# Kernel tuning notes

Hardware: AMD Instinct MI355X
Metric: run time of the kernel (lower is better)

The kernel has to match this reference:

```python
import jax, jax.numpy as jnp
import numpy as np

H = 16
HEAD_DIM = 64
LORA_RANK = 32
LORA_ALPHA = 1.0


def _lora_linear(x, W, A, B):
    # torch Linear: y = x @ W.T ; LoRA side path: x @ A @ B * (alpha/rank)
    return x @ W.T + (x @ A) @ B * (LORA_ALPHA / LORA_RANK)


def setup_inputs() -> dict:
    key = jax.random.key(0)
    ks = jax.random.split(key, 8)
    B, S, D = 2, 2048, 1024
    x = jax.random.normal(ks[0], (B, S, D), dtype=jnp.float32)
    # ALiBi-style bias per head with causal mask baked in (combined bias)
    alibi_bias = jax.random.normal(ks[1], (H, S, S), dtype=jnp.float32)
    pad_mask = jnp.zeros((B, 1, 1, S), dtype=jnp.float32)
    W_qkv = jax.random.normal(ks[2], (3 * D, D), dtype=jnp.float32) * 0.02
    A_qkv = jax.random.normal(ks[3], (D, LORA_RANK), dtype=jnp.float32) * 0.02
    B_qkv = jax.random.normal(ks[4], (LORA_RANK, 3 * D), dtype=jnp.float32) * 0.02
    W_out = jax.random.normal(ks[5], (D, D), dtype=jnp.float32) * 0.02
    A_out = jax.random.normal(ks[6], (D, LORA_RANK), dtype=jnp.float32) * 0.02
    B_out = jax.random.normal(ks[7], (LORA_RANK, D), dtype=jnp.float32) * 0.02
    return {"x": x, "alibi_bias": alibi_bias, "pad_mask": pad_mask,
            "W_qkv": W_qkv, "A_qkv": A_qkv, "B_qkv": B_qkv,
            "W_out": W_out, "A_out": A_out, "B_out": B_out}


def reference(x, alibi_bias, pad_mask, W_qkv, A_qkv, B_qkv, W_out, A_out, B_out):
    Bsz, S, D = x.shape
    qkv = _lora_linear(x, W_qkv, A_qkv, B_qkv)              # [B,S,3D]
    qkv = qkv.reshape(Bsz, S, 3, H, HEAD_DIM)
    q = jnp.transpose(qkv[:, :, 0], (0, 2, 1, 3))           # [B,H,S,hd]
    k = jnp.transpose(qkv[:, :, 1], (0, 2, 1, 3))
    v = jnp.transpose(qkv[:, :, 2], (0, 2, 1, 3))
    scores = jnp.einsum('bhqd,bhkd->bhqk', q, k) / jnp.sqrt(jnp.float32(HEAD_DIM))
    scores = scores + alibi_bias[None] + pad_mask           # [B,H,S,S]
    weights = jax.nn.softmax(scores, axis=-1)
    # dropout: eval mode (training=False) -> identity
    attn = jnp.einsum('bhqk,bhkd->bhqd', weights, v)        # [B,H,S,hd]
    attn = jnp.transpose(attn, (0, 2, 1, 3)).reshape(Bsz, S, D)
    return _lora_linear(attn, W_out, A_out, B_out)
```

## Files before the change

kernel.cpp:

```cpp
#include <hip/hip_runtime.h>

#define H_ 16
#define HD_ 64
#define S_ 2048
#define D_ 1024
#define B_ 2
#define R_ 32
#define M_ 4096
#define N3_ 3072

typedef __attribute__((ext_vector_type(8))) short short8;
typedef __attribute__((ext_vector_type(4))) float f32x4;
typedef unsigned short u16;
typedef __attribute__((ext_vector_type(4))) unsigned short u16x4;

__device__ inline u16 f2bf(float f) {
  unsigned u = __float_as_uint(f);
  u += 0x7fff + ((u >> 16) & 1);
  return (u16)(u >> 16);
}

__global__ void fold_kernel(const float* __restrict__ W,
                            const float* __restrict__ A,
                            const float* __restrict__ Bm,
                            u16* __restrict__ out, int OUT, int IN) {
  int idx = blockIdx.x * 256 + threadIdx.x;
  int o = idx / IN;
  int i = idx - o * IN;
  float s = 0.f;
#pragma unroll
  for (int r = 0; r < R_; ++r) s += A[i * R_ + r] * Bm[r * OUT + o];
  out[idx] = f2bf(W[idx] + s * (1.0f / 32.0f));
}

__global__ void cvt_kernel(const float* __restrict__ x, u16* __restrict__ xb) {
  int i = (blockIdx.x * 256 + threadIdx.x) * 4;
  const float4 v = *(const float4*)(x + i);
  u16x4 o = {f2bf(v.x), f2bf(v.y), f2bf(v.z), f2bf(v.w)};
  *(u16x4*)(xb + i) = o;
}

template <int EPI>
__global__ __launch_bounds__(256) void gemm_bf16(
    const u16* __restrict__ X, const u16* __restrict__ Wb,
    float* __restrict__ Yf, u16* __restrict__ Qb, u16* __restrict__ Kb,
    u16* __restrict__ Vtb, int M, int N, int K) {
  __shared__ u16 As[128][40];
  __shared__ u16 Bs[128][40];
  const int t = threadIdx.x;
  const int lane = t & 63;
  const int w = t >> 6;
  const int quad = lane >> 4;
  const int l = lane & 15;
  const int wh = w >> 1;
  const int ww = w & 1;
  const int bm = blockIdx.y * 128;
  const int bn = blockIdx.x * 128;
  const int srow = t >> 1;
  const int soff = (t & 1) * 16;
  const u16* Xp = X + (size_t)(bm + srow) * K + soff;
  const u16* Wp = Wb + (size_t)(bn + srow) * K + soff;
  f32x4 acc[4][4];
#pragma unroll
  for (int i = 0; i < 4; ++i)
#pragma unroll
    for (int j = 0; j < 4; ++j) acc[i][j] = (f32x4){0.f, 0.f, 0.f, 0.f};

  for (int k0 = 0; k0 < K; k0 += 32) {
    const short8 xa = *(const short8*)(Xp + k0);
    const short8 xc = *(const short8*)(Xp + k0 + 8);
    const short8 wa = *(const short8*)(Wp + k0);
    const short8 wc = *(const short8*)(Wp + k0 + 8);
    __syncthreads();
    *(short8*)&As[srow][soff] = xa;
    *(short8*)&As[srow][soff + 8] = xc;
    *(short8*)&Bs[srow][soff] = wa;
    *(short8*)&Bs[srow][soff + 8] = wc;
    __syncthreads();
    short8 af[4], bf[4];
#pragma unroll
    for (int mt = 0; mt < 4; ++mt)
      af[mt] = *(const short8*)&As[wh * 64 + mt * 16 + l][quad * 8];
#pragma unroll
    for (int nt = 0; nt < 4; ++nt)
      bf[nt] = *(const short8*)&Bs[ww * 64 + nt * 16 + l][quad * 8];
#pragma unroll
    for (int mt = 0; mt < 4; ++mt)
#pragma unroll
      for (int nt = 0; nt < 4; ++nt)
        acc[mt][nt] = __builtin_amdgcn_mfma_f32_16x16x32_bf16(
            af[mt], bf[nt], acc[mt][nt], 0, 0, 0);
  }
#pragma unroll
  for (int mt = 0; mt < 4; ++mt) {
#pragma unroll
    for (int nt = 0; nt < 4; ++nt) {
      const int m0 = bm + wh * 64 + mt * 16 + quad * 4;
      const int n = bn + ww * 64 + nt * 16 + l;
      if (EPI == 0) {
#pragma unroll
        for (int r = 0; r < 4; ++r)
          Yf[(size_t)(m0 + r) * N + n] = acc[mt][nt][r];
      } else {
        const int b = m0 >> 11;
        const int s0 = m0 & 2047;
        const int part = n >> 10;
        const int h = (n & 1023) >> 6;
        const int d = n & 63;
        if (part == 0) {
#pragma unroll
          for (int r = 0; r < 4; ++r)
            Qb[((size_t)(b * 16 + h) * 2048 + s0 + r) * 64 + d] =
                f2bf(acc[mt][nt][r]);
        } else if (part == 1) {
#pragma unroll
          for (int r = 0; r < 4; ++r)
            Kb[((size_t)(b * 16 + h) * 2048 + s0 + r) * 64 + d] =
                f2bf(acc[mt][nt][r]);
        } else {
          u16x4 pv = {f2bf(acc[mt][nt][0]), f2bf(acc[mt][nt][1]),
                      f2bf(acc[mt][nt][2]), f2bf(acc[mt][nt][3])};
          *(u16x4*)(Vtb + ((size_t)(b * 16 + h) * 64 + d) * 2048 + s0) = pv;
        }
      }
    }
  }
}

__global__ __launch_bounds__(256) void attn_mfma(
    const u16* __restrict__ Qb, const u16* __restrict__ Kb,
    const u16* __restrict__ Vtb, const float* __restrict__ alibi,
    const float* __restrict__ pad, u16* __restrict__ ctxb) {
  __shared__ u16 KL[64][72];
  __shared__ u16 VL[64][72];
  __shared__ u16 PL[4][32][72];
  const int t = threadIdx.x;
  const int lane = t & 63;
  const int w = t >> 6;
  const int quad = lane >> 4;
  const int l = lane & 15;
  const int b = blockIdx.x;
  const int q0 = blockIdx.y * 128;
  const int h = blockIdx.z;
  const int bh = b * 16 + h;
  const int srow = t >> 2;
  const int sq = (t & 3) * 16;

  short8 qf[2][2];
#pragma unroll
  for (int mt = 0; mt < 2; ++mt)
#pragma unroll
    for (int kq = 0; kq < 2; ++kq)
      qf[mt][kq] = *(const short8*)(Qb +
          ((size_t)bh * 2048 + q0 + w * 32 + mt * 16 + l) * 64 + kq * 32 +
          quad * 8);

  f32x4 Ou[2][4];
  float mrun[2][4], lrun[2][4];
#pragma unroll
  for (int mt = 0; mt < 2; ++mt) {
#pragma unroll
    for (int r = 0; r < 4; ++r) { mrun[mt][r] = -1e30f; lrun[mt][r] = 0.f; }
#pragma unroll
    for (int dn = 0; dn < 4; ++dn) Ou[mt][dn] = (f32x4){0.f, 0.f, 0.f, 0.f};
  }

  const u16* Kg = Kb + ((size_t)bh * 2048) * 64;
  const u16* Vg = Vtb + ((size_t)bh * 64) * 2048;

  for (int kt = 0; kt < S_ / 64; ++kt) {
    const int k0 = kt * 64;
    const short8 kv0 = *(const short8*)(Kg + (size_t)(k0 + srow) * 64 + sq);
    const short8 kv1 = *(const short8*)(Kg + (size_t)(k0 + srow) * 64 + sq + 8);
    const short8 vv0 = *(const short8*)(Vg + (size_t)srow * 2048 + k0 + sq);
    const short8 vv1 = *(const short8*)(Vg + (size_t)srow * 2048 + k0 + sq + 8);
    __syncthreads();
    *(short8*)&KL[srow][sq] = kv0;
    *(short8*)&KL[srow][sq + 8] = kv1;
    *(short8*)&VL[srow][sq] = vv0;
    *(short8*)&VL[srow][sq + 8] = vv1;
    __syncthreads();

    short8 kf[4][2];
#pragma unroll
    for (int nt = 0; nt < 4; ++nt)
#pragma unroll
      for (int kq = 0; kq < 2; ++kq)
        kf[nt][kq] = *(const short8*)&KL[nt * 16 + l][kq * 32 + quad * 8];
    f32x4 sc[2][4];
#pragma unroll
    for (int mt = 0; mt < 2; ++mt)
#pragma unroll
      for (int nt = 0; nt < 4; ++nt) {
        f32x4 c = {0.f, 0.f, 0.f, 0.f};
        c = __builtin_amdgcn_mfma_f32_16x16x32_bf16(qf[mt][0], kf[nt][0], c, 0, 0, 0);
        c = __builtin_amdgcn_mfma_f32_16x16x32_bf16(qf[mt][1], kf[nt][1], c, 0, 0, 0);
        sc[mt][nt] = c;
      }

    float padv[4];
#pragma unroll
    for (int nt = 0; nt < 4; ++nt) padv[nt] = pad[(size_t)b * S_ + k0 + nt * 16 + l];
#pragma unroll
    for (int mt = 0; mt < 2; ++mt)
#pragma unroll
      for (int nt = 0; nt < 4; ++nt) {
        const float* ap = alibi +
            ((size_t)h * S_ + q0 + w * 32 + mt * 16 + quad * 4) * S_ + k0 +
            nt * 16 + l;
#pragma unroll
        for (int r = 0; r < 4; ++r)
          sc[mt][nt][r] = fmaf(sc[mt][nt][r], 0.125f,
                               ap[(size_t)r * S_] + padv[nt]);
      }

#pragma unroll
    for (int mt = 0; mt < 2; ++mt) {
#pragma unroll
      for (int r = 0; r < 4; ++r) {
        float rm = fmaxf(fmaxf(sc[mt][0][r], sc[mt][1][r]),
                         fmaxf(sc[mt][2][r], sc[mt][3][r]));
#pragma unroll
        for (int off = 1; off < 16; off <<= 1)
          rm = fmaxf(rm, __shfl_xor(rm, off, 16));
        const float mnew = fmaxf(mrun[mt][r], rm);
        const float alpha = __expf(mrun[mt][r] - mnew);
        mrun[mt][r] = mnew;
        float rs = 0.f;
#pragma unroll
        for (int nt = 0; nt < 4; ++nt) {
          const float e = __expf(sc[mt][nt][r] - mnew);
          sc[mt][nt][r] = e;
          rs += e;
        }
#pragma unroll
        for (int off = 1; off < 16; off <<= 1) rs += __shfl_xor(rs, off, 16);
        lrun[mt][r] = lrun[mt][r] * alpha + rs;
#pragma unroll
        for (int dn = 0; dn < 4; ++dn) Ou[mt][dn][r] *= alpha;
      }
    }

#pragma unroll
    for (int mt = 0; mt < 2; ++mt)
#pragma unroll
      for (int nt = 0; nt < 4; ++nt)
#pragma unroll
        for (int r = 0; r < 4; ++r)
          PL[w][mt * 16 + quad * 4 + r][nt * 16 + l] = f2bf(sc[mt][nt][r]);

    short8 vf[4][2], pf[2][2];
#pragma unroll
    for (int dn = 0; dn < 4; ++dn)
#pragma unroll
      for (int kq = 0; kq < 2; ++kq)
        vf[dn][kq] = *(const short8*)&VL[dn * 16 + l][kq * 32 + quad * 8];
#pragma unroll
    for (int mt = 0; mt < 2; ++mt)
#pragma unroll
      for (int kq = 0; kq < 2; ++kq)
        pf[mt][kq] = *(const short8*)&PL[w][mt * 16 + l][kq * 32 + quad * 8];
#pragma unroll
    for (int mt = 0; mt < 2; ++mt)
#pragma unroll
      for (int dn = 0; dn < 4; ++dn) {
        Ou[mt][dn] = __builtin_amdgcn_mfma_f32_16x16x32_bf16(
            pf[mt][0], vf[dn][0], Ou[mt][dn], 0, 0, 0);
        Ou[mt][dn] = __builtin_amdgcn_mfma_f32_16x16x32_bf16(
            pf[mt][1], vf[dn][1], Ou[mt][dn], 0, 0, 0);
      }
  }

#pragma unroll
  for (int mt = 0; mt < 2; ++mt) {
#pragma unroll
    for (int r = 0; r < 4; ++r) {
      const float inv = 1.0f / lrun[mt][r];
      const int s = q0 + w * 32 + mt * 16 + quad * 4 + r;
#pragma unroll
      for (int dn = 0; dn < 4; ++dn)
        ctxb[((size_t)b * 2048 + s) * 1024 + h * 64 + dn * 16 + l] =
            f2bf(Ou[mt][dn][r] * inv);
    }
  }
}

extern "C" void kernel_launch(void* const* d_in, const int* in_sizes, int n_in,
                              void* d_out, int out_size, void* d_ws,
                              size_t ws_size, hipStream_t stream) {
  const float* x     = (const float*)d_in[0];
  const float* alibi = (const float*)d_in[1];
  const float* pad   = (const float*)d_in[2];
  const float* W_qkv = (const float*)d_in[3];
  const float* A_qkv = (const float*)d_in[4];
  const float* B_qkv = (const float*)d_in[5];
  const float* W_out = (const float*)d_in[6];
  const float* A_out = (const float*)d_in[7];
  const float* B_out = (const float*)d_in[8];
  float* out = (float*)d_out;

  u16* ws = (u16*)d_ws;
  u16* xb    = ws;
  u16* weffq = xb + (size_t)M_ * D_;
  u16* weffo = weffq + (size_t)N3_ * D_;
  u16* Qb    = weffo + (size_t)D_ * D_;
  u16* Kb    = Qb + (size_t)M_ * D_;
  u16* Vtb   = Kb + (size_t)M_ * D_;
  u16* ctxb  = Vtb + (size_t)M_ * D_;

  fold_kernel<<<(N3_ * D_) / 256, 256, 0, stream>>>(W_qkv, A_qkv, B_qkv, weffq,
                                                    N3_, D_);
  fold_kernel<<<(D_ * D_) / 256, 256, 0, stream>>>(W_out, A_out, B_out, weffo,
                                                   D_, D_);
  cvt_kernel<<<(M_ * D_) / 1024, 256, 0, stream>>>(x, xb);
  gemm_bf16<1><<<dim3(N3_ / 128, M_ / 128), 256, 0, stream>>>(
      xb, weffq, nullptr, Qb, Kb, Vtb, M_, N3_, D_);
  attn_mfma<<<dim3(B_, S_ / 128, H_), 256, 0, stream>>>(Qb, Kb, Vtb, alibi,
                                                        pad, ctxb);
  gemm_bf16<0><<<dim3(D_ / 128, M_ / 128), 256, 0, stream>>>(
      ctxb, weffo, out, nullptr, nullptr, nullptr, M_, D_, D_);
}
```

Before: 625.8 us.

## Share alibi loads across batches in attention and use direct global-to-LDS loads in GEMM

The attention kernel now gives each block both batch elements for one head and a 64-query tile, so each alibi value is loaded once and reused for both batches. Alibi for the next key tile is prefetched into registers. K and V are read straight from global memory into registers instead of being staged through shared memory, which removes the per-tile barriers. The GEMM now uses global_load_lds to copy tiles into unpadded shared memory, which may add LDS bank conflicts on the fragment reads, and without LDS staging each wave reloads the same K/V tile, raising global/cache traffic.

Result: slower. 732.4 us (+17.0%).

```diff
diff --git a/kernel.cpp b/kernel.cpp
--- a/kernel.cpp
+++ b/kernel.cpp
@@ -20,6 +20,12 @@
   return (u16)(u >> 16);
 }
 
+__device__ __forceinline__ void glds16(const u16* g, u16* lds) {
+  __builtin_amdgcn_global_load_lds(
+      (const __attribute__((address_space(1))) unsigned int*)g,
+      (__attribute__((address_space(3))) unsigned int*)lds, 16, 0, 0);
+}
+
 __global__ void fold_kernel(const float* __restrict__ W,
                             const float* __restrict__ A,
                             const float* __restrict__ Bm,
@@ -45,8 +51,8 @@
     const u16* __restrict__ X, const u16* __restrict__ Wb,
     float* __restrict__ Yf, u16* __restrict__ Qb, u16* __restrict__ Kb,
     u16* __restrict__ Vtb, int M, int N, int K) {
-  __shared__ u16 As[128][40];
-  __shared__ u16 Bs[128][40];
+  __shared__ u16 As[128 * 32];
+  __shared__ u16 Bs[128 * 32];
   const int t = threadIdx.x;
   const int lane = t & 63;
   const int w = t >> 6;
@@ -56,10 +62,16 @@
   const int ww = w & 1;
   const int bm = blockIdx.y * 128;
   const int bn = blockIdx.x * 128;
-  const int srow = t >> 1;
-  const int soff = (t & 1) * 16;
-  const u16* Xp = X + (size_t)(bm + srow) * K + soff;
-  const u16* Wp = Wb + (size_t)(bn + srow) * K + soff;
+  const int srow0 = 2 * w * 16 + (lane >> 2);
+  const int scol = (lane & 3) * 8;
+  const u16* gA = X + (size_t)(bm + srow0) * K + scol;
+  const u16* gB = Wb + (size_t)(bn + srow0) * K + scol;
+  const size_t segK = (size_t)16 * K;
+  u16* lA0 = As + 2 * w * 512;
+  u16* lA1 = lA0 + 512;
+  u16* lB0 = Bs + 2 * w * 512;
+  u16* lB1 = lB0 + 512;
+
   f32x4 acc[4][4];
 #pragma unroll
   for (int i = 0; i < 4; ++i)
@@ -67,23 +79,19 @@
     for (int j = 0; j < 4; ++j) acc[i][j] = (f32x4){0.f, 0.f, 0.f, 0.f};
 
   for (int k0 = 0; k0 < K; k0 += 32) {
-    const short8 xa = *(const short8*)(Xp + k0);
-    const short8 xc = *(const short8*)(Xp + k0 + 8);
-    const short8 wa = *(const short8*)(Wp + k0);
-    const short8 wc = *(const short8*)(Wp + k0 + 8);
     __syncthreads();
-    *(short8*)&As[srow][soff] = xa;
-    *(short8*)&As[srow][soff + 8] = xc;
-    *(short8*)&Bs[srow][soff] = wa;
-    *(short8*)&Bs[srow][soff + 8] = wc;
+    glds16(gA + k0, lA0);
+    glds16(gA + k0 + segK, lA1);
+    glds16(gB + k0, lB0);
+    glds16(gB + k0 + segK, lB1);
     __syncthreads();
     short8 af[4], bf[4];
 #pragma unroll
     for (int mt = 0; mt < 4; ++mt)
-      af[mt] = *(const short8*)&As[wh * 64 + mt * 16 + l][quad * 8];
+      af[mt] = *(const short8*)&As[(wh * 64 + mt * 16 + l) * 32 + quad * 8];
 #pragma unroll
     for (int nt = 0; nt < 4; ++nt)
-      bf[nt] = *(const short8*)&Bs[ww * 64 + nt * 16 + l][quad * 8];
+      bf[nt] = *(const short8*)&Bs[(ww * 64 + nt * 16 + l) * 32 + quad * 8];
 #pragma unroll
     for (int mt = 0; mt < 4; ++mt)
 #pragma unroll
@@ -131,158 +139,153 @@
     const u16* __restrict__ Qb, const u16* __restrict__ Kb,
     const u16* __restrict__ Vtb, const float* __restrict__ alibi,
     const float* __restrict__ pad, u16* __restrict__ ctxb) {
-  __shared__ u16 KL[64][72];
-  __shared__ u16 VL[64][72];
-  __shared__ u16 PL[4][32][72];
+  __shared__ u16 PL[4][16][72];
   const int t = threadIdx.x;
   const int lane = t & 63;
   const int w = t >> 6;
   const int quad = lane >> 4;
   const int l = lane & 15;
-  const int b = blockIdx.x;
-  const int q0 = blockIdx.y * 128;
-  const int h = blockIdx.z;
-  const int bh = b * 16 + h;
-  const int srow = t >> 2;
-  const int sq = (t & 3) * 16;
+  const int q0 = blockIdx.x * 64;
+  const int h = blockIdx.y;
+  const int qw = q0 + w * 16;
 
   short8 qf[2][2];
 #pragma unroll
-  for (int mt = 0; mt < 2; ++mt)
+  for (int b = 0; b < 2; ++b)
 #pragma unroll
     for (int kq = 0; kq < 2; ++kq)
-      qf[mt][kq] = *(const short8*)(Qb +
-          ((size_t)bh * 2048 + q0 + w * 32 + mt * 16 + l) * 64 + kq * 32 +
+      qf[b][kq] = *(const short8*)(
+          Qb + ((size_t)(b * 16 + h) * 2048 + qw + l) * 64 + kq * 32 +
           quad * 8);
 
   f32x4 Ou[2][4];
   float mrun[2][4], lrun[2][4];
 #pragma unroll
-  for (int mt = 0; mt < 2; ++mt) {
-#pragma unroll
-    for (int r = 0; r < 4; ++r) { mrun[mt][r] = -1e30f; lrun[mt][r] = 0.f; }
-#pragma unroll
-    for (int dn = 0; dn < 4; ++dn) Ou[mt][dn] = (f32x4){0.f, 0.f, 0.f, 0.f};
+  for (int b = 0; b < 2; ++b) {
+#pragma unroll
+    for (int r = 0; r < 4; ++r) { mrun[b][r] = -1e30f; lrun[b][r] = 0.f; }
+#pragma unroll
+    for (int dn = 0; dn < 4; ++dn) Ou[b][dn] = (f32x4){0.f, 0.f, 0.f, 0.f};
   }
 
-  const u16* Kg = Kb + ((size_t)bh * 2048) * 64;
-  const u16* Vg = Vtb + ((size_t)bh * 64) * 2048;
+  const float* ap0 = alibi + ((size_t)h * S_ + qw + quad * 4) * S_ + l;
+  float alc[4][4];
+#pragma unroll
+  for (int nt = 0; nt < 4; ++nt)
+#pragma unroll
+    for (int r = 0; r < 4; ++r)
+      alc[nt][r] = ap0[(size_t)r * S_ + nt * 16];
+
+  const u16* Kg0 = Kb + (size_t)h * 2048 * 64;
+  const u16* Vg0 = Vtb + (size_t)h * 64 * 2048;
+  const size_t bstride = (size_t)16 * 2048 * 64;
 
   for (int kt = 0; kt < S_ / 64; ++kt) {
     const int k0 = kt * 64;
-    const short8 kv0 = *(const short8*)(Kg + (size_t)(k0 + srow) * 64 + sq);
-    const short8 kv1 = *(const short8*)(Kg + (size_t)(k0 + srow) * 64 + sq + 8);
-    const short8 vv0 = *(const short8*)(Vg + (size_t)srow * 2048 + k0 + sq);
-    const short8 vv1 = *(const short8*)(Vg + (size_t)srow * 2048 + k0 + sq + 8);
-    __syncthreads();
-    *(short8*)&KL[srow][sq] = kv0;
-    *(short8*)&KL[srow][sq + 8] = kv1;
-    *(short8*)&VL[srow][sq] = vv0;
-    *(short8*)&VL[srow][sq + 8] = vv1;
-    __syncthreads();
-
-    short8 kf[4][2];
-#pragma unroll
-    for (int nt = 0; nt < 4; ++nt)
-#pragma unroll
-      for (int kq = 0; kq < 2; ++kq)
-        kf[nt][kq] = *(const short8*)&KL[nt * 16 + l][kq * 32 + quad * 8];
-    f32x4 sc[2][4];
-#pragma unroll
-    for (int mt = 0; mt < 2; ++mt)
+    float aln[4][4];
+    if (kt < S_ / 64 - 1) {
+#pragma unroll
+      for (int nt = 0; nt < 4; ++nt)
+#pragma unroll
+        for (int r = 0; r < 4; ++r)
+          aln[nt][r] = ap0[(size_t)r * S_ + k0 + 64 + nt * 16];
+    }
+    float padv[2][4];
+#pragma unroll
+    for (int b = 0; b < 2; ++b)
+#pragma unroll
+      for (int nt = 0; nt < 4; ++nt)
+        padv[b][nt] = pad[(size_t)b * S_ + k0 + nt * 16 + l];
+
+#pragma unroll
+    for (int b = 0; b < 2; ++b) {
+      const u16* Kg = Kg0 + (size_t)b * bstride + (size_t)k0 * 64;
+      const u16* Vg = Vg0 + (size_t)b * bstride;
+      short8 kf[4][2];
+#pragma unroll
+      for (int nt = 0; nt < 4; ++nt)
+#pragma unroll
+        for (int kq = 0; kq < 2; ++kq)
+          kf[nt][kq] = *(const short8*)(Kg + (size_t)(nt * 16 + l) * 64 +
+                                        kq * 32 + quad * 8);
+      f32x4 sc[4];
 #pragma unroll
       for (int nt = 0; nt < 4; ++nt) {
         f32x4 c = {0.f, 0.f, 0.f, 0.f};
-        c = __builtin_amdgcn_mfma_f32_16x16x32_bf16(qf[mt][0], kf[nt][0], c, 0, 0, 0);
-        c = __builtin_amdgcn_mfma_f32_16x16x32_bf16(qf[mt][1], kf[nt][1], c, 0, 0, 0);
-        sc[mt][nt] = c;
+        c = __builtin_amdgcn_mfma_f32_16x16x32_bf16(qf[b][0], kf[nt][0], c, 0, 0, 0);
+        c = __builtin_amdgcn_mfma_f32_16x16x32_bf16(qf[b][1], kf[nt][1], c, 0, 0, 0);
+        sc[nt] = c;
       }
-
-    float padv[4];
-#pragma unroll
-    for (int nt = 0; nt < 4; ++nt) padv[nt] = pad[(size_t)b * S_ + k0 + nt * 16 + l];
-#pragma unroll
-    for (int mt = 0; mt < 2; ++mt)
-#pragma unroll
-      for (int nt = 0; nt < 4; ++nt) {
-        const float* ap = alibi +
-            ((size_t)h * S_ + q0 + w * 32 + mt * 16 + quad * 4) * S_ + k0 +
-            nt * 16 + l;
+#pragma unroll
+      for (int nt = 0; nt < 4; ++nt)
 #pragma unroll
         for (int r = 0; r < 4; ++r)
-          sc[mt][nt][r] = fmaf(sc[mt][nt][r], 0.125f,
-                               ap[(size_t)r * S_] + padv[nt]);
-      }
-
-#pragma unroll
-    for (int mt = 0; mt < 2; ++mt) {
+          sc[nt][r] = fmaf(sc[nt][r], 0.125f, alc[nt][r] + padv[b][nt]);
 #pragma unroll
       for (int r = 0; r < 4; ++r) {
-        float rm = fmaxf(fmaxf(sc[mt][0][r], sc[mt][1][r]),
-                         fmaxf(sc[mt][2][r], sc[mt][3][r]));
+        float rm = fmaxf(fmaxf(sc[0][r], sc[1][r]), fmaxf(sc[2][r], sc[3][r]));
 #pragma unroll
         for (int off = 1; off < 16; off <<= 1)
           rm = fmaxf(rm, __shfl_xor(rm, off, 16));
-        const float mnew = fmaxf(mrun[mt][r], rm);
-        const float alpha = __expf(mrun[mt][r] - mnew);
-        mrun[mt][r] = mnew;
+        const float mnew = fmaxf(mrun[b][r], rm);
+        const float alpha = __expf(mrun[b][r] - mnew);
+        mrun[b][r] = mnew;
         float rs = 0.f;
 #pragma unroll
         for (int nt = 0; nt < 4; ++nt) {
-          const float e = __expf(sc[mt][nt][r] - mnew);
-          sc[mt][nt][r] = e;
+          const float e = __expf(sc[nt][r] - mnew);
+          sc[nt][r] = e;
           rs += e;
         }
 #pragma unroll
         for (int off = 1; off < 16; off <<= 1) rs += __shfl_xor(rs, off, 16);
-        lrun[mt][r] = lrun[mt][r] * alpha + rs;
-#pragma unroll
-        for (int dn = 0; dn < 4; ++dn) Ou[mt][dn][r] *= alpha;
+        lrun[b][r] = lrun[b][r] * alpha + rs;
+#pragma unroll
+        for (int dn = 0; dn < 4; ++dn) Ou[b][dn][r] *= alpha;
       }
-    }
-
-#pragma unroll
-    for (int mt = 0; mt < 2; ++mt)
 #pragma unroll
       for (int nt = 0; nt < 4; ++nt)
 #pragma unroll
         for (int r = 0; r < 4; ++r)
-          PL[w][mt * 16 + quad * 4 + r][nt * 16 + l] = f2bf(sc[mt][nt][r]);
-
-    short8 vf[4][2], pf[2][2];
-#pragma unroll
-    for (int dn = 0; dn < 4; ++dn)
+          PL[w][quad * 4 + r][nt * 16 + l] = f2bf(sc[nt][r]);
+      short8 vf[4][2];
+#pragma unroll
+      for (int dn = 0; dn < 4; ++dn)
+#pragma unroll
+        for (int kq = 0; kq < 2; ++kq)
+          vf[dn][kq] = *(const short8*)(Vg + (size_t)(dn * 16 + l) * 2048 +
+                                        k0 + kq * 32 + quad * 8);
+      short8 pf[2];
 #pragma unroll
       for (int kq = 0; kq < 2; ++kq)
-        vf[dn][kq] = *(const short8*)&VL[dn * 16 + l][kq * 32 + quad * 8];
-#pragma unroll
-    for (int mt = 0; mt < 2; ++mt)
-#pragma unroll
-      for (int kq = 0; kq < 2; ++kq)
-        pf[mt][kq] = *(const short8*)&PL[w][mt * 16 + l][kq * 32 + quad * 8];
-#pragma unroll
-    for (int mt = 0; mt < 2; ++mt)
+        pf[kq] = *(const short8*)&PL[w][l][kq * 32 + quad * 8];
 #pragma unroll
       for (int dn = 0; dn < 4; ++dn) {
-        Ou[mt][dn] = __builtin_amdgcn_mfma_f32_16x16x32_bf16(
-            pf[mt][0], vf[dn][0], Ou[mt][dn], 0, 0, 0);
-        Ou[mt][dn] = __builtin_amdgcn_mfma_f32_16x16x32_bf16(
-            pf[mt][1], vf[dn][1], Ou[mt][dn], 0, 0, 0);
+        Ou[b][dn] = __builtin_amdgcn_mfma_f32_16x16x32_bf16(
+            pf[0], vf[dn][0], Ou[b][dn], 0, 0, 0);
+        Ou[b][dn] = __builtin_amdgcn_mfma_f32_16x16x32_bf16(
+            pf[1], vf[dn][1], Ou[b][dn], 0, 0, 0);
       }
+    }
+    if (kt < S_ / 64 - 1) {
+#pragma unroll
+      for (int nt = 0; nt < 4; ++nt)
+#pragma unroll
+        for (int r = 0; r < 4; ++r) alc[nt][r] = aln[nt][r];
+    }
   }
 
 #pragma unroll
-  for (int mt = 0; mt < 2; ++mt) {
+  for (int b = 0; b < 2; ++b)
 #pragma unroll
     for (int r = 0; r < 4; ++r) {
-      const float inv = 1.0f / lrun[mt][r];
-      const int s = q0 + w * 32 + mt * 16 + quad * 4 + r;
+      const float inv = 1.0f / lrun[b][r];
+      const int s = qw + quad * 4 + r;
 #pragma unroll
       for (int dn = 0; dn < 4; ++dn)
         ctxb[((size_t)b * 2048 + s) * 1024 + h * 64 + dn * 16 + l] =
-            f2bf(Ou[mt][dn][r] * inv);
-    }
-  }
+            f2bf(Ou[b][dn][r] * inv);
+    }
 }
 
 extern "C" void kernel_launch(void* const* d_in, const int* in_sizes, int n_in,
@@ -315,8 +318,8 @@
   cvt_kernel<<<(M_ * D_) / 1024, 256, 0, stream>>>(x, xb);
   gemm_bf16<1><<<dim3(N3_ / 128, M_ / 128), 256, 0, stream>>>(
       xb, weffq, nullptr, Qb, Kb, Vtb, M_, N3_, D_);
-  attn_mfma<<<dim3(B_, S_ / 128, H_), 256, 0, stream>>>(Qb, Kb, Vtb, alibi,
-                                                        pad, ctxb);
+  attn_mfma<<<dim3(S_ / 64, H_), 256, 0, stream>>>(Qb, Kb, Vtb, alibi, pad,
+                                                   ctxb);
   gemm_bf16<0><<<dim3(D_ / 128, M_ / 128), 256, 0, stream>>>(
       ctxb, weffo, out, nullptr, nullptr, nullptr, M_, D_, D_);
 }
```
